# Kernel tuning notes

Hardware: AMD Instinct MI355X
Metric: run time of the kernel (lower is better)

The kernel has to match this reference:

```python
import jax, jax.numpy as jnp
import numpy as np
import math

FACTOR = 5

def setup_inputs() -> dict:
    key = jax.random.key(0)
    k1, k2, k3, k4 = jax.random.split(key, 4)
    B, L, H, D = 4, 2048, 8, 64
    sample_k = FACTOR * math.ceil(math.log(L))  # 40
    queries = jax.random.normal(k1, (B, L, H, D), dtype=jnp.float32)
    keys = jax.random.normal(k2, (B, L, H, D), dtype=jnp.float32)
    values = jax.random.normal(k3, (B, L, H, D), dtype=jnp.float32)
    index_sample = jax.random.randint(k4, (L, sample_k), 0, L, dtype=jnp.int32)
    return {"queries": queries, "keys": keys, "values": values, "index_sample": index_sample}

def reference(queries, keys, values, index_sample):
    B, L_Q, H, D = queries.shape
    L_K = keys.shape[1]
    # [B,L,H,D] -> [B,H,L,D]
    Q = jnp.swapaxes(queries, 1, 2)
    K = jnp.swapaxes(keys, 1, 2)
    # values are cumsum'ed along the length axis before attention
    Vc = jnp.cumsum(jnp.swapaxes(values, 1, 2), axis=-2)
    u = min(FACTOR * math.ceil(math.log(L_Q)), L_Q)  # n_top
    # --- _prob_QK ---
    # gather sampled keys per query position: [B,H,L_Q,sample_k,D]
    K_sample = K[:, :, index_sample, :]
    # sampled scores: [B,H,L_Q,sample_k]
    Q_K_sample = jnp.einsum('bhqd,bhqsd->bhqs', Q, K_sample)
    # sparsity measure M = max - mean(scaled by L_K)
    M = Q_K_sample.max(axis=-1) - Q_K_sample.sum(axis=-1) / L_K  # [B,H,L_Q]
    M_top = jax.lax.top_k(M, u)[1]  # [B,H,u] query indices
    # gather top queries: [B,H,u,D]
    Q_reduce = jnp.take_along_axis(Q, M_top[..., None], axis=2)
    # full scores for selected queries: [B,H,u,L_K]
    scores = jnp.einsum('bhud,bhkd->bhuk', Q_reduce, K)
    scale = 1.0 / math.sqrt(D)
    scores = scores * scale
    # mask_flag=False, output_attention=False -> plain softmax then matmul with cumsum'ed V
    attn = jax.nn.softmax(scores, axis=-1)
    context = jnp.einsum('bhuk,bhkd->bhud', attn, Vc)  # [B,H,u,D]
    return context
```

## Files before the change

### kernel.cpp

```cpp
#include <hip/hip_runtime.h>
#include <hip/hip_bf16.h>
#include <math.h>

#define B 4
#define L 2048
#define H 8
#define D 64
#define SK 40
#define U 40
#define JC 32
#define JCL (L / JC)

#define OFF_M    0
#define OFF_TOP  262144
#define OFF_T    270336
#define OFF_PART 10756096

__device__ __forceinline__ float dot4(float4 a, float4 b) {
    return fmaf(a.x, b.x, fmaf(a.y, b.y, fmaf(a.z, b.z, a.w * b.w)));
}

__global__ __launch_bounds__(256) void k_msamp(const float* __restrict__ Q,
                                               const float* __restrict__ K,
                                               const int* __restrict__ idx,
                                               float* __restrict__ M) {
    int g  = blockIdx.x & 7;
    int b  = g >> 1;
    int hh = g & 1;
    int t  = threadIdx.x;
    int q  = (blockIdx.x >> 3) * 4 + (t >> 6);
    int c  = t & 15;
    int hp = (t >> 4) & 3;
    int h  = hh * 4 + hp;

    float4 q4 = *((const float4*)(Q + (size_t)((b * L + q) * H + h) * D) + c);

    const int* ip = idx + q * SK;
    const float* kbase = K + (size_t)b * L * H * D + (size_t)h * D + c * 4;

    float vmax = -__builtin_inff();
    float vsum = 0.f;
#pragma unroll 8
    for (int s = 0; s < SK; ++s) {
        int kidx = ip[s];
        float4 k4 = *(const float4*)(kbase + (size_t)kidx * (H * D));
        float d4 = dot4(q4, k4);
        d4 += __shfl_xor(d4, 1, 64);
        d4 += __shfl_xor(d4, 2, 64);
        d4 += __shfl_xor(d4, 4, 64);
        d4 += __shfl_xor(d4, 8, 64);
        vmax = fmaxf(vmax, d4);
        vsum += d4;
    }
    if (c == 0) M[(size_t)(b * H + h) * L + q] = vmax - vsum * (1.0f / (float)L);
}

__global__ __launch_bounds__(256) void k_topk(const float* __restrict__ M,
                                              int* __restrict__ top) {
    __shared__ unsigned long long cand[L];
    __shared__ unsigned int bins[256];
    __shared__ unsigned int red[256];
    __shared__ int cnt2;

    int bh = blockIdx.x;
    int tid = threadIdx.x;
    const float* m = M + (size_t)bh * L;

    bins[tid] = 0;
    if (tid == 0) cnt2 = 0;

    unsigned int u8[8];
    unsigned int umin = 0xFFFFFFFFu, umax = 0u;
#pragma unroll
    for (int e = 0; e < 8; ++e) {
        int i = tid * 8 + e;
        unsigned int bits = __float_as_uint(m[i]);
        unsigned int u = (bits & 0x80000000u) ? ~bits : (bits | 0x80000000u);
        u8[e] = u;
        umin = min(umin, u);
        umax = max(umax, u);
    }
    red[tid] = umin;
    __syncthreads();
    for (int s = 128; s; s >>= 1) {
        if (tid < s) red[tid] = min(red[tid], red[tid + s]);
        __syncthreads();
    }
    unsigned int kmin = red[0];
    __syncthreads();
    red[tid] = umax;
    __syncthreads();
    for (int s = 128; s; s >>= 1) {
        if (tid < s) red[tid] = max(red[tid], red[tid + s]);
        __syncthreads();
    }
    unsigned int kmax = red[0];
    __syncthreads();

    unsigned int range = kmax - kmin;
    if (range == 0u) {
        if (tid < U) top[bh * U + tid] = tid;
        return;
    }
    int hb = 31 - __clz(range);
    int shift = (hb > 7) ? (hb - 7) : 0;

#pragma unroll
    for (int e = 0; e < 8; ++e) {
        unsigned int bin = (u8[e] - kmin) >> shift;
        atomicAdd(&bins[bin], 1u);
    }
    __syncthreads();

    red[tid] = bins[tid];
    __syncthreads();
    for (int s = 1; s < 256; s <<= 1) {
        unsigned int add = (tid + s < 256) ? red[tid + s] : 0u;
        __syncthreads();
        red[tid] += add;
        __syncthreads();
    }
    int cnt = __syncthreads_count(red[tid] >= U);
    unsigned int t = (unsigned int)(cnt - 1);

#pragma unroll
    for (int e = 0; e < 8; ++e) {
        unsigned int u = u8[e];
        if (((u - kmin) >> shift) >= t) {
            int pos = atomicAdd(&cnt2, 1);
            int i = tid * 8 + e;
            cand[pos] = ((unsigned long long)u << 11) | (unsigned long long)(2047 - i);
        }
    }
    __syncthreads();
    int C = cnt2;

    for (int j = tid; j < C; j += 256) {
        unsigned long long kj = cand[j];
        int r = 0;
        for (int kk = 0; kk < C; ++kk) r += (cand[kk] > kj);
        if (r < U) top[bh * U + r] = 2047 - (int)(kj & 0x7FFull);
    }
}

__global__ __launch_bounds__(256) void k_scores(const float* __restrict__ Q,
                                                const float* __restrict__ K,
                                                const int* __restrict__ top,
                                                float* __restrict__ T) {
    __shared__ float4 sQ4[U * 16];
    int bh = blockIdx.x >> 4;
    int kc = blockIdx.x & 15;
    int b = bh >> 3, h = bh & (H - 1);
    int tid = threadIdx.x;
    int lane = tid & 63;
    int w = tid >> 6;

    for (int i = tid; i < U * 16; i += 256) {
        int u = i >> 4, c = i & 15;
        int qidx = top[bh * U + u];
        sQ4[i] = *((const float4*)(Q + (size_t)((b * L + qidx) * H + h) * D) + c);
    }

    int k0 = kc * 128 + lane;
    const float4* kr0 = (const float4*)(K + (size_t)((b * L + k0) * H + h) * D);
    const float4* kr1 = (const float4*)(K + (size_t)((b * L + k0 + 64) * H + h) * D);
    float4 kv0[16], kv1[16];
#pragma unroll
    for (int i = 0; i < 16; ++i) { kv0[i] = kr0[i]; kv1[i] = kr1[i]; }
    __syncthreads();

    float* Tb = T + (size_t)bh * U * L;
    for (int uu = 0; uu < 10; ++uu) {
        int u = w * 10 + uu;
        float s0 = 0.f, s1 = 0.f;
#pragma unroll
        for (int i = 0; i < 16; ++i) {
            float4 q4 = sQ4[u * 16 + i];
            s0 += dot4(q4, kv0[i]);
            s1 += dot4(q4, kv1[i]);
        }
        Tb[(size_t)u * L + k0]      = s0 * 0.125f;
        Tb[(size_t)u * L + k0 + 64] = s1 * 0.125f;
    }
}

__global__ __launch_bounds__(256) void k_softsuf(float* __restrict__ T) {
    __shared__ float red[256];
    __shared__ float arr[256];
    int row = blockIdx.x;
    float* t = T + (size_t)row * L;
    int tid = threadIdx.x;

    const float4* p = (const float4*)(t + tid * 8);
    float4 a = p[0], c = p[1];
    float x[8] = {a.x, a.y, a.z, a.w, c.x, c.y, c.z, c.w};

    float mx = x[0];
#pragma unroll
    for (int i = 1; i < 8; ++i) mx = fmaxf(mx, x[i]);
    red[tid] = mx;
    __syncthreads();
    for (int s = 128; s; s >>= 1) {
        if (tid < s) red[tid] = fmaxf(red[tid], red[tid + s]);
        __syncthreads();
    }
    float maxv = red[0];
    __syncthreads();

    float e[8];
#pragma unroll
    for (int i = 0; i < 8; ++i) e[i] = __expf(x[i] - maxv);
    float ls[8];
    ls[7] = e[7];
#pragma unroll
    for (int i = 6; i >= 0; --i) ls[i] = e[i] + ls[i + 1];
    float mytotal = ls[0];

    arr[tid] = mytotal;
    __syncthreads();
    for (int s = 1; s < 256; s <<= 1) {
        float add = (tid + s < 256) ? arr[tid + s] : 0.f;
        __syncthreads();
        arr[tid] += add;
        __syncthreads();
    }
    float denom = arr[0];
    float off = arr[tid] - mytotal;
    float r = 1.0f / denom;

    float4 o0 = make_float4((ls[0] + off) * r, (ls[1] + off) * r,
                            (ls[2] + off) * r, (ls[3] + off) * r);
    float4 o1 = make_float4((ls[4] + off) * r, (ls[5] + off) * r,
                            (ls[6] + off) * r, (ls[7] + off) * r);
    float4* po = (float4*)(t + tid * 8);
    po[0] = o0; po[1] = o1;
}

__global__ __launch_bounds__(256) void k_ctx(const float* __restrict__ V,
                                             const float* __restrict__ T,
                                             float* __restrict__ part) {
    __shared__ float4 sT4[U * (JCL / 4)];
    int bh = blockIdx.x >> 5;
    int jc = blockIdx.x & 31;
    int b = bh >> 3, h = bh & (H - 1);
    int tid = threadIdx.x;
    int d = tid & 63;
    int w = tid >> 6;

    const float4* Tg = (const float4*)(T + (size_t)bh * U * L);
    for (int i = tid; i < U * (JCL / 4); i += 256) {
        int u = i >> 4;
        int c = i & 15;
        sT4[i] = Tg[u * (L / 4) + jc * (JCL / 4) + c];
    }
    __syncthreads();

    float acc[10];
#pragma unroll
    for (int uu = 0; uu < 10; ++uu) acc[uu] = 0.f;

    const float* Vb = V + (size_t)b * L * H * D + (size_t)h * D + d;
#pragma unroll 2
    for (int jj = 0; jj < JCL / 4; ++jj) {
        int j0 = jc * JCL + jj * 4;
        float v0 = Vb[(size_t)(j0 + 0) * (H * D)];
        float v1 = Vb[(size_t)(j0 + 1) * (H * D)];
        float v2 = Vb[(size_t)(j0 + 2) * (H * D)];
        float v3 = Vb[(size_t)(j0 + 3) * (H * D)];
#pragma unroll
        for (int uu = 0; uu < 10; ++uu) {
            float4 t4 = sT4[(w * 10 + uu) * 16 + jj];
            acc[uu] = fmaf(t4.x, v0, fmaf(t4.y, v1, fmaf(t4.z, v2, fmaf(t4.w, v3, acc[uu]))));
        }
    }

    float* po = part + ((size_t)jc * (B * H) + bh) * (U * D);
#pragma unroll
    for (int uu = 0; uu < 10; ++uu) po[(w * 10 + uu) * D + d] = acc[uu];
}

__global__ __launch_bounds__(256) void k_red(const float* __restrict__ part,
                                             float* __restrict__ out) {
    int o = blockIdx.x * 256 + threadIdx.x;
    if (o >= B * H * U * D) return;
    int bh = o / (U * D);
    int rest = o - bh * (U * D);
    float s = 0.f;
#pragma unroll
    for (int jc = 0; jc < JC; ++jc)
        s += part[(size_t)(jc * (B * H) + bh) * (U * D) + rest];
    out[o] = s;
}

extern "C" void kernel_launch(void* const* d_in, const int* in_sizes, int n_in,
                              void* d_out, int out_size, void* d_ws, size_t ws_size,
                              hipStream_t stream) {
    const float* Q  = (const float*)d_in[0];
    const float* K  = (const float*)d_in[1];
    const float* V  = (const float*)d_in[2];
    const int* idx  = (const int*)d_in[3];
    float* out = (float*)d_out;

    float* M    = (float*)((char*)d_ws + OFF_M);
    int*   top  = (int*)  ((char*)d_ws + OFF_TOP);
    float* T    = (float*)((char*)d_ws + OFF_T);
    float* part = (float*)((char*)d_ws + OFF_PART);

    k_msamp<<<(L / 4) * 8, 256, 0, stream>>>(Q, K, idx, M);
    k_topk<<<B * H, 256, 0, stream>>>(M, top);
    k_scores<<<B * H * 16, 256, 0, stream>>>(Q, K, top, T);
    k_softsuf<<<B * H * U, 256, 0, stream>>>(T);
    k_ctx<<<B * H * JC, 256, 0, stream>>>(V, T, part);
    k_red<<<(B * H * U * D + 255) / 256, 256, 0, stream>>>(part, out);
}
```

Baseline: 162.9 us.

## Widen per-lane loads in sampling and context kernels with shuffle-distributed indices

The sampled-score kernel now gives each lane 8 floats (two float4) per key row, so each wave covers two queries with four heads, and it halves the grid. The sample indices are loaded once per lane and broadcast with shuffles rather than reloaded every iteration. The context kernel now loads V as float4 across four j positions per wave and reduces over j with cross-lane shuffles before a float4 store. The aim is fewer, wider memory transactions and fewer reduction shuffles, at the cost of extra shuffle work and more registers.

```diff
diff --git a/kernel.cpp b/kernel.cpp
--- a/kernel.cpp
+++ b/kernel.cpp
@@ -28,29 +28,40 @@
     int b  = g >> 1;
     int hh = g & 1;
     int t  = threadIdx.x;
-    int q  = (blockIdx.x >> 3) * 4 + (t >> 6);
-    int c  = t & 15;
-    int hp = (t >> 4) & 3;
+    int wave = t >> 6;
+    int lane = t & 63;
+    int qp = lane >> 5;
+    int hp = (lane >> 3) & 3;
+    int c  = lane & 7;
     int h  = hh * 4 + hp;
-
-    float4 q4 = *((const float4*)(Q + (size_t)((b * L + q) * H + h) * D) + c);
-
-    const int* ip = idx + q * SK;
-    const float* kbase = K + (size_t)b * L * H * D + (size_t)h * D + c * 4;
+    int q  = (blockIdx.x >> 3) * 8 + wave * 2 + qp;
+
+    const float* qrow = Q + (size_t)((b * L + q) * H + h) * D + c * 8;
+    float4 qa = *(const float4*)qrow;
+    float4 qb = *(const float4*)(qrow + 4);
+
+    int s1 = lane & 31;
+    int v1 = idx[q * SK + s1];
+    int s2 = 32 + s1; if (s2 > SK - 1) s2 = SK - 1;
+    int v2 = idx[q * SK + s2];
+
+    const float* kbase = K + (size_t)b * L * H * D + (size_t)h * D + c * 8;
 
     float vmax = -__builtin_inff();
     float vsum = 0.f;
 #pragma unroll 8
     for (int s = 0; s < SK; ++s) {
-        int kidx = ip[s];
-        float4 k4 = *(const float4*)(kbase + (size_t)kidx * (H * D));
-        float d4 = dot4(q4, k4);
-        d4 += __shfl_xor(d4, 1, 64);
-        d4 += __shfl_xor(d4, 2, 64);
-        d4 += __shfl_xor(d4, 4, 64);
-        d4 += __shfl_xor(d4, 8, 64);
-        vmax = fmaxf(vmax, d4);
-        vsum += d4;
+        int kidx = (s < 32) ? __shfl(v1, qp * 32 + s, 64)
+                            : __shfl(v2, qp * 32 + (s - 32), 64);
+        const float* kp = kbase + (size_t)kidx * (H * D);
+        float4 ka = *(const float4*)kp;
+        float4 kb = *(const float4*)(kp + 4);
+        float d8 = dot4(qa, ka) + dot4(qb, kb);
+        d8 += __shfl_xor(d8, 1, 64);
+        d8 += __shfl_xor(d8, 2, 64);
+        d8 += __shfl_xor(d8, 4, 64);
+        vmax = fmaxf(vmax, d8);
+        vsum += d8;
     }
     if (c == 0) M[(size_t)(b * H + h) * L + q] = vmax - vsum * (1.0f / (float)L);
 }
@@ -239,44 +250,53 @@
 __global__ __launch_bounds__(256) void k_ctx(const float* __restrict__ V,
                                              const float* __restrict__ T,
                                              float* __restrict__ part) {
-    __shared__ float4 sT4[U * (JCL / 4)];
+    __shared__ float sT[U][JCL];
     int bh = blockIdx.x >> 5;
     int jc = blockIdx.x & 31;
     int b = bh >> 3, h = bh & (H - 1);
     int tid = threadIdx.x;
-    int d = tid & 63;
     int w = tid >> 6;
-
-    const float4* Tg = (const float4*)(T + (size_t)bh * U * L);
+    int lane = tid & 63;
+    int j2 = lane >> 4;
+    int d4 = lane & 15;
+
+    const float* Tg = T + (size_t)bh * U * L + jc * JCL;
+    float4* sT4 = (float4*)sT;
     for (int i = tid; i < U * (JCL / 4); i += 256) {
-        int u = i >> 4;
-        int c = i & 15;
-        sT4[i] = Tg[u * (L / 4) + jc * (JCL / 4) + c];
-    }
-    __syncthreads();
-
-    float acc[10];
-#pragma unroll
-    for (int uu = 0; uu < 10; ++uu) acc[uu] = 0.f;
-
-    const float* Vb = V + (size_t)b * L * H * D + (size_t)h * D + d;
-#pragma unroll 2
-    for (int jj = 0; jj < JCL / 4; ++jj) {
-        int j0 = jc * JCL + jj * 4;
-        float v0 = Vb[(size_t)(j0 + 0) * (H * D)];
-        float v1 = Vb[(size_t)(j0 + 1) * (H * D)];
-        float v2 = Vb[(size_t)(j0 + 2) * (H * D)];
-        float v3 = Vb[(size_t)(j0 + 3) * (H * D)];
+        int u = i >> 4, cc = i & 15;
+        sT4[i] = ((const float4*)(Tg + (size_t)u * L))[cc];
+    }
+    __syncthreads();
+
+    float4 acc[10];
+#pragma unroll
+    for (int uu = 0; uu < 10; ++uu) acc[uu] = make_float4(0.f, 0.f, 0.f, 0.f);
+
+    const float* Vb = V + (size_t)(b * L) * (H * D) + (size_t)h * D + d4 * 4;
+#pragma unroll 4
+    for (int it = 0; it < JCL / 4; ++it) {
+        int j = it * 4 + j2;
+        float4 v4 = *(const float4*)(Vb + (size_t)(jc * JCL + j) * (H * D));
 #pragma unroll
         for (int uu = 0; uu < 10; ++uu) {
-            float4 t4 = sT4[(w * 10 + uu) * 16 + jj];
-            acc[uu] = fmaf(t4.x, v0, fmaf(t4.y, v1, fmaf(t4.z, v2, fmaf(t4.w, v3, acc[uu]))));
+            float tj = sT[w * 10 + uu][j];
+            acc[uu].x = fmaf(tj, v4.x, acc[uu].x);
+            acc[uu].y = fmaf(tj, v4.y, acc[uu].y);
+            acc[uu].z = fmaf(tj, v4.z, acc[uu].z);
+            acc[uu].w = fmaf(tj, v4.w, acc[uu].w);
         }
     }
 
     float* po = part + ((size_t)jc * (B * H) + bh) * (U * D);
 #pragma unroll
-    for (int uu = 0; uu < 10; ++uu) po[(w * 10 + uu) * D + d] = acc[uu];
+    for (int uu = 0; uu < 10; ++uu) {
+        float4 a = acc[uu];
+        a.x += __shfl_xor(a.x, 16, 64); a.y += __shfl_xor(a.y, 16, 64);
+        a.z += __shfl_xor(a.z, 16, 64); a.w += __shfl_xor(a.w, 16, 64);
+        a.x += __shfl_xor(a.x, 32, 64); a.y += __shfl_xor(a.y, 32, 64);
+        a.z += __shfl_xor(a.z, 32, 64); a.w += __shfl_xor(a.w, 32, 64);
+        if (j2 == 0) *(float4*)(po + (w * 10 + uu) * D + d4 * 4) = a;
+    }
 }
 
 __global__ __launch_bounds__(256) void k_red(const float* __restrict__ part,
@@ -306,7 +326,7 @@
     float* T    = (float*)((char*)d_ws + OFF_T);
     float* part = (float*)((char*)d_ws + OFF_PART);
 
-    k_msamp<<<(L / 4) * 8, 256, 0, stream>>>(Q, K, idx, M);
+    k_msamp<<<(L / 8) * 8, 256, 0, stream>>>(Q, K, idx, M);
     k_topk<<<B * H, 256, 0, stream>>>(M, top);
     k_scores<<<B * H * 16, 256, 0, stream>>>(Q, K, top, T);
     k_softsuf<<<B * H * U, 256, 0, stream>>>(T);
```

Measured after the change: 156.5 us. -3.9%, faster.
